# Performance work log

Hardware: AMD Instinct MI355X
Metric: run time of the kernel (lower is better)

Reference implementation:

```python
import jax, jax.numpy as jnp
import numpy as np

N_NODES, N_EDGES, F_IN, HID, N_CLASSES = 50000, 800000, 128, 128, 10
HEADS, D_HEAD, N_GRAPHS, N_CONV = 4, 32, 256, 3
BN_EPS = 1e-5
NEG_SLOPE = 0.2


def batchnorm(x, g, b):
    # training-mode BN: batch mean / biased variance over dim 0
    m = x.mean(axis=0)
    v = x.var(axis=0)
    return (x - m) * jax.lax.rsqrt(v + BN_EPS) * g + b


def segment_softmax(logits, seg, n):
    # numerically stable softmax over edges grouped by destination node
    m = jax.ops.segment_max(logits, seg, num_segments=n)
    e = jnp.exp(logits - m[seg])
    s = jax.ops.segment_sum(e, seg, num_segments=n)
    return e / (s[seg] + 1e-16)


def gat_conv(x, src, dst, W, a_src, a_dst, bias):
    # PyG GATConv (concat=True), eval mode (no attention dropout)
    n = x.shape[0]
    h = (x @ W).reshape(n, HEADS, D_HEAD)                 # [N,H,Dh]
    al_s = jnp.einsum('nhd,hd->nh', h, a_src)             # alpha from source
    al_d = jnp.einsum('nhd,hd->nh', h, a_dst)             # alpha from dest
    logits = jax.nn.leaky_relu(al_s[src] + al_d[dst], NEG_SLOPE)   # [E,H]
    alpha = segment_softmax(logits, dst, n)                # softmax over incoming edges
    msg = h[src] * alpha[:, :, None]                       # [E,H,Dh]
    out = jax.ops.segment_sum(msg, dst, num_segments=n)    # [N,H,Dh]
    return out.reshape(n, HEADS * D_HEAD) + bias


def setup_inputs() -> dict:
    key = jax.random.key(0)
    ks = jax.random.split(key, 12)
    s = 0.05
    inp = {
        'x': jax.random.normal(ks[0], (N_NODES, F_IN), dtype=jnp.float32),
        'edge_index': jax.random.randint(ks[1], (2, N_EDGES), 0, N_NODES, dtype=jnp.int32),
        'batch': jnp.sort(jax.random.randint(ks[2], (N_NODES,), 0, N_GRAPHS, dtype=jnp.int32)),
        # GCNConv(gfn=True): plain weight, no bias used
        'w_feat': s * jax.random.normal(ks[3], (F_IN, HID), dtype=jnp.float32),
        'bnf_g': jnp.ones((F_IN,), jnp.float32),
        'bnf_b': jnp.full((F_IN,), 1e-4, jnp.float32),
        'bnc_g': jnp.ones((N_CONV, HID), jnp.float32),
        'bnc_b': jnp.full((N_CONV, HID), 1e-4, jnp.float32),
        'gat_w': s * jax.random.normal(ks[4], (N_CONV, HID, HID), dtype=jnp.float32),
        'gat_asrc': s * jax.random.normal(ks[5], (N_CONV, HEADS, D_HEAD), dtype=jnp.float32),
        'gat_adst': s * jax.random.normal(ks[6], (N_CONV, HEADS, D_HEAD), dtype=jnp.float32),
        'gat_b': jnp.zeros((N_CONV, HID), jnp.float32),
        'bnfc_g': jnp.ones((HID,), jnp.float32),
        'bnfc_b': jnp.full((HID,), 1e-4, jnp.float32),
        'lin_w': s * jax.random.normal(ks[7], (HID, HID), dtype=jnp.float32),
        'lin_b': jnp.zeros((HID,), jnp.float32),
        'bnh_g': jnp.ones((HID,), jnp.float32),
        'bnh_b': jnp.full((HID,), 1e-4, jnp.float32),
        'cls_w': s * jax.random.normal(ks[8], (HID, N_CLASSES), dtype=jnp.float32),
        'cls_b': jnp.zeros((N_CLASSES,), jnp.float32),
    }
    return inp


def reference(x, edge_index, batch, w_feat, bnf_g, bnf_b, bnc_g, bnc_b,
              gat_w, gat_asrc, gat_adst, gat_b, bnfc_g, bnfc_b,
              lin_w, lin_b, bnh_g, bnh_b, cls_w, cls_b):
    n = x.shape[0]
    loops = jnp.arange(n, dtype=edge_index.dtype)
    src = jnp.concatenate([edge_index[0], loops])   # self-loops (PyG GATConv default)
    dst = jnp.concatenate([edge_index[1], loops])

    h = jax.nn.relu(batchnorm(x, bnf_g, bnf_b) @ w_feat)   # bn_feat + gfn GCNConv + relu
    for i in range(N_CONV):
        h = batchnorm(h, bnc_g[i], bnc_b[i])
        h = jax.nn.relu(gat_conv(h, src, dst, gat_w[i], gat_asrc[i], gat_adst[i], gat_b[i]))

    g = jax.ops.segment_sum(h, batch, num_segments=N_GRAPHS)   # global_add_pool [G,HID]
    g = jax.nn.relu(batchnorm(g, bnfc_g, bnfc_b) @ lin_w + lin_b)
    g = batchnorm(g, bnh_g, bnh_b)
    # dropout inactive in eval mode
    return jax.nn.log_softmax(g @ cls_w + cls_b, axis=-1)
```

## Files before the change

### kernel.cpp

```cpp
#include <hip/hip_runtime.h>
#include <math.h>

#define N_NODES 50000
#define N_EDGES 800000
#define NGRAPHS 256
#define NCONV 3
#define SCAT_CHUNK 2048
#define DMAX 64

typedef _Float16 h4 __attribute__((ext_vector_type(4)));
typedef _Float16 h8 __attribute__((ext_vector_type(8)));
typedef float f32x4 __attribute__((ext_vector_type(4)));

static inline int divup(int a, int b) { return (a + b - 1) / b; }

#define SB_CONV 0
#define SB_H2 2048
#define SB_X 2304
#define SB_TOT 2560

#define NSCAT_BLOCKS 3128

__global__ void init_kernel(float* __restrict__ SB, int* __restrict__ cursor,
                            int* __restrict__ col, int n) {
    int i = blockIdx.x * blockDim.x + threadIdx.x;
    if (i < SB_TOT) SB[i] = 0.f;
    if (i < n) {
        cursor[i] = 1;
        col[(size_t)i * DMAX] = i;
    }
}

__global__ __launch_bounds__(256) void scatter_cast(const int* __restrict__ src,
                                                    const int* __restrict__ dst,
                                                    int* __restrict__ cursor,
                                                    int* __restrict__ col, int E,
                                                    const float* __restrict__ x,
                                                    _Float16* __restrict__ y, int n,
                                                    float* __restrict__ sums) {
    if ((int)blockIdx.x < NSCAT_BLOCKS) {
        int slice = blockIdx.x & 7;
        int base = (blockIdx.x >> 3) * SCAT_CHUNK;
        int lim = min(base + SCAT_CHUNK, E);
        int lo = slice * (N_NODES / 8);
        int hi = lo + (N_NODES / 8);
        for (int i = base + threadIdx.x; i < lim; i += 256) {
            int d = dst[i];
            if (d >= lo && d < hi) {
                int p = atomicAdd(&cursor[d], 1);
                if (p < DMAX) col[(size_t)d * DMAX + p] = src[i];
            }
        }
        return;
    }
    __shared__ float S[16][128], S2[16][128];
    int bid = blockIdx.x - NSCAT_BLOCKS;
    int tid = threadIdx.x;
    int c8 = (tid & 15) * 8;
    int rg = tid >> 4;
    float s[8] = {}, s2[8] = {};
    for (int r = bid * 16 + rg; r < n; r += 256 * 16) {
        const float4* p = (const float4*)&x[(size_t)r * 128 + c8];
        float4 v0 = p[0], v1 = p[1];
        float f[8] = {v0.x, v0.y, v0.z, v0.w, v1.x, v1.y, v1.z, v1.w};
        h8 o;
#pragma unroll
        for (int i = 0; i < 8; ++i) {
            o[i] = (_Float16)f[i];
            s[i] += f[i];
            s2[i] += f[i] * f[i];
        }
        *(h8*)&y[(size_t)r * 128 + c8] = o;
    }
#pragma unroll
    for (int i = 0; i < 8; ++i) { S[rg][c8 + i] = s[i]; S2[rg][c8 + i] = s2[i]; }
    __syncthreads();
    if (tid < 128) {
        float a = 0.f, b = 0.f;
#pragma unroll
        for (int k = 0; k < 16; ++k) { a += S[k][tid]; b += S2[k][tid]; }
        atomicAdd(&sums[tid], a);
        atomicAdd(&sums[128 + tid], b);
    }
}

__global__ __launch_bounds__(256) void colstats_h(const _Float16* __restrict__ x, int n,
                                                  float* __restrict__ sums) {
    __shared__ float S[16][128], S2[16][128];
    int tid = threadIdx.x;
    int c8 = (tid & 15) * 8;
    int rg = tid >> 4;
    float s[8] = {}, s2[8] = {};
    for (int r = blockIdx.x * 16 + rg; r < n; r += gridDim.x * 16) {
        h8 v = *(const h8*)&x[(size_t)r * 128 + c8];
#pragma unroll
        for (int i = 0; i < 8; ++i) {
            float f = (float)v[i];
            s[i] += f;
            s2[i] += f * f;
        }
    }
#pragma unroll
    for (int i = 0; i < 8; ++i) { S[rg][c8 + i] = s[i]; S2[rg][c8 + i] = s2[i]; }
    __syncthreads();
    if (tid < 128) {
        float a = 0.f, b = 0.f;
#pragma unroll
        for (int k = 0; k < 16; ++k) { a += S[k][tid]; b += S2[k][tid]; }
        atomicAdd(&sums[(blockIdx.x & 7) * 256 + tid], a);
        atomicAdd(&sums[(blockIdx.x & 7) * 256 + 128 + tid], b);
    }
}

__global__ __launch_bounds__(128) void fold_t(const float* __restrict__ sums, int nsl,
                                              float inv_n,
                                              const float* __restrict__ gamma,
                                              const float* __restrict__ beta,
                                              const float* __restrict__ W,
                                              _Float16* __restrict__ WTh, float* __restrict__ bp) {
    int j = blockIdx.x, k = threadIdx.x;
    float s1 = 0.f, s2v = 0.f;
    for (int s = 0; s < nsl; ++s) { s1 += sums[s * 256 + k]; s2v += sums[s * 256 + 128 + k]; }
    float mean = s1 * inv_n;
    float var = s2v * inv_n - mean * mean;
    float sc = gamma[k] * rsqrtf(var + 1e-5f);
    float t = beta[k] - mean * sc;
    float w = W[k * 128 + j];
    WTh[j * 128 + k] = (_Float16)(sc * w);
    float pb = t * w;
    for (int off = 1; off < 64; off <<= 1) pb += __shfl_xor(pb, off, 64);
    __shared__ float r2[2];
    if ((k & 63) == 0) r2[k >> 6] = pb;
    __syncthreads();
    if (k == 0) bp[j] = r2[0] + r2[1];
}

__global__ __launch_bounds__(256) void gemm_mfma(const _Float16* __restrict__ Ah,
                                                 const _Float16* __restrict__ WTh,
                                                 const float* __restrict__ bp,
                                                 _Float16* __restrict__ outh, int n, int relu,
                                                 const float* __restrict__ asrc,
                                                 const float* __restrict__ adst,
                                                 float* __restrict__ als,
                                                 float* __restrict__ ald,
                                                 float* __restrict__ stats8,
                                                 float* __restrict__ sums_zero,
                                                 float* __restrict__ g_zero) {
    __shared__ _Float16 Wl[128 * 136];
    __shared__ float SSm[4 * 128], SS2m[4 * 128];
    int tid = threadIdx.x;
    if (sums_zero && blockIdx.x < 8) sums_zero[blockIdx.x * 256 + tid] = 0.f;
    if (g_zero && blockIdx.x < 128) g_zero[blockIdx.x * 256 + tid] = 0.f;
    for (int i = tid; i < 2048; i += 256) {
        int r = i >> 4, s = i & 15;
        *(h8*)&Wl[r * 136 + s * 8] = *(const h8*)&WTh[r * 128 + s * 8];
    }
    __syncthreads();
    int lane = tid & 63, wid = tid >> 6;
    int m = lane & 15, quad = lane >> 4;
    int rbase = blockIdx.x * 64 + wid * 16;
    bool act = rbase < n;
    const bool do_al = (asrc != nullptr);
    const bool do_st = (stats8 != nullptr);
    float st[8] = {}, s2t[8] = {};
    float ps[4][4] = {}, pd[4][4] = {};

    if (act) {
        const _Float16* arow = Ah + (size_t)(rbase + m) * 128 + quad * 8;
        h8 af0 = *(const h8*)(arow);
        h8 af1 = *(const h8*)(arow + 32);
        h8 af2 = *(const h8*)(arow + 64);
        h8 af3 = *(const h8*)(arow + 96);
#pragma unroll
        for (int t = 0; t < 8; ++t) {
            const _Float16* wrow = &Wl[(t * 16 + m) * 136 + quad * 8];
            f32x4 acc = {0.f, 0.f, 0.f, 0.f};
            acc = __builtin_amdgcn_mfma_f32_16x16x32_f16(af0, *(const h8*)(wrow), acc, 0, 0, 0);
            acc = __builtin_amdgcn_mfma_f32_16x16x32_f16(af1, *(const h8*)(wrow + 32), acc, 0, 0, 0);
            acc = __builtin_amdgcn_mfma_f32_16x16x32_f16(af2, *(const h8*)(wrow + 64), acc, 0, 0, 0);
            acc = __builtin_amdgcn_mfma_f32_16x16x32_f16(af3, *(const h8*)(wrow + 96), acc, 0, 0, 0);
            int j = t * 16 + m;
            float bj = bp[j];
            float avs = 0.f, avd = 0.f;
            if (do_al) { avs = asrc[j]; avd = adst[j]; }
            int hh = t >> 1;
#pragma unroll
            for (int r = 0; r < 4; ++r) {
                float o = acc[r] + bj;
                if (do_al) {
                    ps[r][hh] += o * avs;
                    pd[r][hh] += o * avd;
                }
                float v = relu ? fmaxf(o, 0.f) : o;
                _Float16 hv16 = (_Float16)v;
                int row = rbase + quad * 4 + r;
                outh[(size_t)row * 128 + j] = hv16;
                if (do_st) {
                    float fv = (float)hv16;
                    st[t] += fv;
                    s2t[t] += fv * fv;
                }
            }
        }
        if (do_al) {
#pragma unroll
            for (int r = 0; r < 4; ++r) {
#pragma unroll
                for (int hh = 0; hh < 4; ++hh) {
                    float v = ps[r][hh];
                    v += __shfl_xor(v, 1, 64); v += __shfl_xor(v, 2, 64);
                    v += __shfl_xor(v, 4, 64); v += __shfl_xor(v, 8, 64);
                    float w = pd[r][hh];
                    w += __shfl_xor(w, 1, 64); w += __shfl_xor(w, 2, 64);
                    w += __shfl_xor(w, 4, 64); w += __shfl_xor(w, 8, 64);
                    if (m == 0) {
                        int row = rbase + quad * 4 + r;
                        als[row * 4 + hh] = v;
                        ald[row * 4 + hh] = w;
                    }
                }
            }
        }
    }
    if (do_st) {
#pragma unroll
        for (int t = 0; t < 8; ++t) {
            st[t] += __shfl_xor(st[t], 16, 64);  st[t] += __shfl_xor(st[t], 32, 64);
            s2t[t] += __shfl_xor(s2t[t], 16, 64); s2t[t] += __shfl_xor(s2t[t], 32, 64);
        }
        if (quad == 0) {
#pragma unroll
            for (int t = 0; t < 8; ++t) {
                SSm[wid * 128 + t * 16 + m] = st[t];
                SS2m[wid * 128 + t * 16 + m] = s2t[t];
            }
        }
        __syncthreads();
        int c = tid & 127, which = tid >> 7;
        const float* A = which ? SS2m : SSm;
        float tot = A[c] + A[128 + c] + A[256 + c] + A[384 + c];
        atomicAdd(&stats8[(blockIdx.x & 7) * 256 + which * 128 + c], tot);
    }
}

__device__ __forceinline__ float leaky(float x) { return fmaxf(x, 0.2f * x); }

__global__ __launch_bounds__(256) void gat_aggregate(const _Float16* __restrict__ hp,
                                                     const float* __restrict__ al_s,
                                                     const float* __restrict__ al_d,
                                                     const int* __restrict__ cnt_arr,
                                                     const int* __restrict__ col,
                                                     const float* __restrict__ bias,
                                                     _Float16* __restrict__ h_out, int n) {
    int tid = threadIdx.x;
    int lane = tid & 63, wid = tid >> 6;
    int node = blockIdx.x * 4 + wid;
    int beg = node * DMAX;
    int end = beg + min(cnt_arr[node], DMAX);
    int q = lane >> 4, l4 = lane & 15;
    int head = l4 >> 2;
    int f0 = l4 * 8;
    float adh = al_d[node * 4 + head];
    float ch = leaky(adh);
    const _Float16* hpf = hp + f0;
    int last = end - 1;
    float ws = 0.f;
    float a0 = 0.f, a1 = 0.f, a2 = 0.f, a3 = 0.f, a4 = 0.f, a5 = 0.f, a6 = 0.f, a7 = 0.f;
    for (int e = beg + q; e < end; e += 16) {
        int e1 = e + 4, e2 = e + 8, e3 = e + 12;
        bool v1 = e1 < end, v2 = e2 < end, v3 = e3 < end;
        unsigned s0 = (unsigned)col[e];
        unsigned s1 = (unsigned)col[v1 ? e1 : last];
        unsigned s2 = (unsigned)col[v2 ? e2 : last];
        unsigned s3 = (unsigned)col[v3 ? e3 : last];
        float as0 = al_s[s0 * 4 + head];
        float as1 = al_s[s1 * 4 + head];
        float as2 = al_s[s2 * 4 + head];
        float as3 = al_s[s3 * 4 + head];
        h8 hv0 = *(const h8*)(hpf + (size_t)s0 * 128);
        h8 hv1 = *(const h8*)(hpf + (size_t)s1 * 128);
        h8 hv2 = *(const h8*)(hpf + (size_t)s2 * 128);
        h8 hv3 = *(const h8*)(hpf + (size_t)s3 * 128);
        float w0 = __expf(fminf(leaky(as0 + adh) - ch, 10.f));
        float w1 = v1 ? __expf(fminf(leaky(as1 + adh) - ch, 10.f)) : 0.f;
        float w2 = v2 ? __expf(fminf(leaky(as2 + adh) - ch, 10.f)) : 0.f;
        float w3 = v3 ? __expf(fminf(leaky(as3 + adh) - ch, 10.f)) : 0.f;
        ws += (w0 + w1) + (w2 + w3);
        a0 += (float)hv0[0] * w0 + (float)hv1[0] * w1 + (float)hv2[0] * w2 + (float)hv3[0] * w3;
        a1 += (float)hv0[1] * w0 + (float)hv1[1] * w1 + (float)hv2[1] * w2 + (float)hv3[1] * w3;
        a2 += (float)hv0[2] * w0 + (float)hv1[2] * w1 + (float)hv2[2] * w2 + (float)hv3[2] * w3;
        a3 += (float)hv0[3] * w0 + (float)hv1[3] * w1 + (float)hv2[3] * w2 + (float)hv3[3] * w3;
        a4 += (float)hv0[4] * w0 + (float)hv1[4] * w1 + (float)hv2[4] * w2 + (float)hv3[4] * w3;
        a5 += (float)hv0[5] * w0 + (float)hv1[5] * w1 + (float)hv2[5] * w2 + (float)hv3[5] * w3;
        a6 += (float)hv0[6] * w0 + (float)hv1[6] * w1 + (float)hv2[6] * w2 + (float)hv3[6] * w3;
        a7 += (float)hv0[7] * w0 + (float)hv1[7] * w1 + (float)hv2[7] * w2 + (float)hv3[7] * w3;
    }
#pragma unroll
    for (int off = 16; off <= 32; off <<= 1) {
        ws += __shfl_xor(ws, off, 64);
        a0 += __shfl_xor(a0, off, 64); a1 += __shfl_xor(a1, off, 64);
        a2 += __shfl_xor(a2, off, 64); a3 += __shfl_xor(a3, off, 64);
        a4 += __shfl_xor(a4, off, 64); a5 += __shfl_xor(a5, off, 64);
        a6 += __shfl_xor(a6, off, 64); a7 += __shfl_xor(a7, off, 64);
    }
    if (q == 0) {
        float inv = 1.f / (ws + 1e-16f);
        float4 b0 = *(const float4*)&bias[f0];
        float4 b1 = *(const float4*)&bias[f0 + 4];
        h8 ov;
        ov[0] = (_Float16)fmaxf(a0 * inv + b0.x, 0.f);
        ov[1] = (_Float16)fmaxf(a1 * inv + b0.y, 0.f);
        ov[2] = (_Float16)fmaxf(a2 * inv + b0.z, 0.f);
        ov[3] = (_Float16)fmaxf(a3 * inv + b0.w, 0.f);
        ov[4] = (_Float16)fmaxf(a4 * inv + b1.x, 0.f);
        ov[5] = (_Float16)fmaxf(a5 * inv + b1.y, 0.f);
        ov[6] = (_Float16)fmaxf(a6 * inv + b1.z, 0.f);
        ov[7] = (_Float16)fmaxf(a7 * inv + b1.w, 0.f);
        *(h8*)&h_out[(size_t)node * 128 + f0] = ov;
    }
}

__global__ void pool_kernel(const _Float16* __restrict__ h, const int* __restrict__ batch,
                            float* __restrict__ g, int n, int chunk) {
    int f = threadIdx.x;
    int a = blockIdx.x * chunk;
    if (a >= n) return;
    int b = min(n, a + chunk);
    float acc = 0.f;
    int cur = batch[a];
    for (int i = a; i < b; ++i) {
        int bi = batch[i];
        if (bi != cur) {
            atomicAdd(&g[cur * 128 + f], acc);
            acc = 0.f;
            cur = bi;
        }
        acc += (float)h[(size_t)i * 128 + f];
    }
    atomicAdd(&g[cur * 128 + f], acc);
}

__global__ __launch_bounds__(256) void gemm128_bn(const float* __restrict__ A,
                                                  const float* __restrict__ W,
                                                  const float* __restrict__ bias,
                                                  float inv_n,
                                                  const float* __restrict__ gamma,
                                                  const float* __restrict__ beta,
                                                  float* __restrict__ out,
                                                  float* __restrict__ outstats, int n) {
    __shared__ float Wl[128 * 128];
    __shared__ float hT[128 * 32];
    __shared__ float S[16][128], S2[16][128];
    __shared__ float sS[128], tS[128];
    int tid = threadIdx.x;
    for (int i = tid; i < 4096; i += 256) {
        ((float4*)Wl)[i] = ((const float4*)W)[i];
    }
    {
        int c8 = (tid & 15) * 8;
        int rg = tid >> 4;
        float s[8] = {}, s2[8] = {};
        for (int r = rg; r < n; r += 16) {
            const float4* p = (const float4*)&A[(size_t)r * 128 + c8];
            float4 v0 = p[0], v1 = p[1];
            float f[8] = {v0.x, v0.y, v0.z, v0.w, v1.x, v1.y, v1.z, v1.w};
#pragma unroll
            for (int i = 0; i < 8; ++i) { s[i] += f[i]; s2[i] += f[i] * f[i]; }
        }
#pragma unroll
        for (int i = 0; i < 8; ++i) { S[rg][c8 + i] = s[i]; S2[rg][c8 + i] = s2[i]; }
    }
    __syncthreads();
    if (tid < 128) {
        float a = 0.f, b2 = 0.f;
#pragma unroll
        for (int k = 0; k < 16; ++k) { a += S[k][tid]; b2 += S2[k][tid]; }
        float m = a * inv_n;
        float var = b2 * inv_n - m * m;
        float sc = gamma[tid] * rsqrtf(var + 1e-5f);
        sS[tid] = sc;
        tS[tid] = beta[tid] - m * sc;
    }
    __syncthreads();
    int base = blockIdx.x * 32;
    for (int pass = 0; pass < 4; ++pass) {
        int r = (tid >> 5) + pass * 8;
        int c4 = tid & 31;
        int row = base + r;
        float4 v = (row < n) ? ((const float4*)(A + (size_t)row * 128))[c4]
                             : make_float4(0.f, 0.f, 0.f, 0.f);
        int c0 = c4 * 4;
        hT[(c0 + 0) * 32 + r] = v.x * sS[c0 + 0] + tS[c0 + 0];
        hT[(c0 + 1) * 32 + r] = v.y * sS[c0 + 1] + tS[c0 + 1];
        hT[(c0 + 2) * 32 + r] = v.z * sS[c0 + 2] + tS[c0 + 2];
        hT[(c0 + 3) * 32 + r] = v.w * sS[c0 + 3] + tS[c0 + 3];
    }
    __syncthreads();
    int tx = tid & 31, ty = tid >> 5;
    int j0 = tx * 4, r0 = ty * 4;
    float acc[4][4] = {};
#pragma unroll 8
    for (int k = 0; k < 128; ++k) {
        float4 a = *(const float4*)&hT[k * 32 + r0];
        float4 w = *(const float4*)&Wl[k * 128 + j0];
        acc[0][0] += a.x * w.x; acc[0][1] += a.x * w.y; acc[0][2] += a.x * w.z; acc[0][3] += a.x * w.w;
        acc[1][0] += a.y * w.x; acc[1][1] += a.y * w.y; acc[1][2] += a.y * w.z; acc[1][3] += a.y * w.w;
        acc[2][0] += a.z * w.x; acc[2][1] += a.z * w.y; acc[2][2] += a.z * w.z; acc[2][3] += a.z * w.w;
        acc[3][0] += a.w * w.x; acc[3][1] += a.w * w.y; acc[3][2] += a.w * w.z; acc[3][3] += a.w * w.w;
    }
    float4 bb = *(const float4*)&bias[j0];
    float csum[4] = {}, csq[4] = {};
    for (int i2 = 0; i2 < 4; ++i2) {
        int row = base + r0 + i2;
        if (row < n) {
            float o0 = fmaxf(acc[i2][0] + bb.x, 0.f);
            float o1 = fmaxf(acc[i2][1] + bb.y, 0.f);
            float o2 = fmaxf(acc[i2][2] + bb.z, 0.f);
            float o3 = fmaxf(acc[i2][3] + bb.w, 0.f);
            *(float4*)&out[(size_t)row * 128 + j0] = make_float4(o0, o1, o2, o3);
            csum[0] += o0; csum[1] += o1; csum[2] += o2; csum[3] += o3;
            csq[0] += o0 * o0; csq[1] += o1 * o1; csq[2] += o2 * o2; csq[3] += o3 * o3;
        }
    }
#pragma unroll
    for (int c = 0; c < 4; ++c) {
        atomicAdd(&outstats[j0 + c], csum[c]);
        atomicAdd(&outstats[128 + j0 + c], csq[c]);
    }
}

__global__ __launch_bounds__(64) void final_kernel(const float* __restrict__ g2,
                                                   const float* __restrict__ stats, float inv_n,
                                                   const float* __restrict__ gamma,
                                                   const float* __restrict__ beta,
                                                   const float* __restrict__ W,
                                                   const float* __restrict__ b,
                                                   float* __restrict__ out, int rows) {
    int r = blockIdx.x;
    if (r >= rows) return;
    int lane = threadIdx.x;
    float logit[10] = {};
    for (int k = lane; k < 128; k += 64) {
        float m = stats[k] * inv_n;
        float var = stats[128 + k] * inv_n - m * m;
        float sc = gamma[k] * rsqrtf(var + 1e-5f);
        float gv = (g2[r * 128 + k] - m) * sc + beta[k];
#pragma unroll
        for (int j = 0; j < 10; ++j) logit[j] += gv * W[k * 10 + j];
    }
#pragma unroll
    for (int j = 0; j < 10; ++j)
        for (int off = 1; off < 64; off <<= 1) logit[j] += __shfl_xor(logit[j], off, 64);
    if (lane == 0) {
        float m = -1e30f;
#pragma unroll
        for (int j = 0; j < 10; ++j) { logit[j] += b[j]; m = fmaxf(m, logit[j]); }
        float sum = 0.f;
#pragma unroll
        for (int j = 0; j < 10; ++j) sum += expf(logit[j] - m);
        float lse = m + logf(sum);
#pragma unroll
        for (int j = 0; j < 10; ++j) out[r * 10 + j] = logit[j] - lse;
    }
}

extern "C" void kernel_launch(void* const* d_in, const int* in_sizes, int n_in,
                              void* d_out, int out_size, void* d_ws, size_t ws_size,
                              hipStream_t stream) {
    const float* x      = (const float*)d_in[0];
    const int*   ei     = (const int*)d_in[1];
    const int*   batch  = (const int*)d_in[2];
    const float* w_feat = (const float*)d_in[3];
    const float* bnf_g  = (const float*)d_in[4];
    const float* bnf_b  = (const float*)d_in[5];
    const float* bnc_g  = (const float*)d_in[6];
    const float* bnc_b  = (const float*)d_in[7];
    const float* gat_w  = (const float*)d_in[8];
    const float* gat_as = (const float*)d_in[9];
    const float* gat_ad = (const float*)d_in[10];
    const float* gat_b  = (const float*)d_in[11];
    const float* bnfc_g = (const float*)d_in[12];
    const float* bnfc_b = (const float*)d_in[13];
    const float* lin_w  = (const float*)d_in[14];
    const float* lin_b  = (const float*)d_in[15];
    const float* bnh_g  = (const float*)d_in[16];
    const float* bnh_b  = (const float*)d_in[17];
    const float* cls_w  = (const float*)d_in[18];
    const float* cls_b  = (const float*)d_in[19];
    float* out = (float*)d_out;

    char* ws = (char*)d_ws;
    size_t off = 0;
    auto alloc = [&](size_t bytes) -> void* {
        void* p = ws + off;
        off = (off + bytes + 255) & ~(size_t)255;
        return p;
    };
    _Float16* xh   = (_Float16*)alloc((size_t)N_NODES * 128 * 2);
    _Float16* h    = (_Float16*)alloc((size_t)N_NODES * 128 * 2);
    _Float16* hp   = (_Float16*)alloc((size_t)N_NODES * 128 * 2);
    float*    als  = (float*)alloc((size_t)N_NODES * 4 * 4);
    float*    ald  = (float*)alloc((size_t)N_NODES * 4 * 4);
    int*      curs = (int*)alloc((size_t)N_NODES * 4);
    int*      col  = (int*)alloc((size_t)N_NODES * DMAX * 4);
    float*    SB   = (float*)alloc(SB_TOT * 4);
    _Float16* WTh  = (_Float16*)alloc(128 * 128 * 2);
    float*    bp   = (float*)alloc(128 * 4);
    float*    g    = (float*)alloc(NGRAPHS * 128 * 4);
    float*    g2   = (float*)alloc(NGRAPHS * 128 * 4);

    const int* esrc = ei;
    const int* edst = ei + N_EDGES;

    init_kernel<<<divup(N_NODES, 256), 256, 0, stream>>>(SB, curs, col, N_NODES);

    scatter_cast<<<NSCAT_BLOCKS + 256, 256, 0, stream>>>(esrc, edst, curs, col, N_EDGES,
                                                         x, xh, N_NODES, SB + SB_X);

    fold_t<<<128, 128, 0, stream>>>(SB + SB_X, 1, 1.f / N_NODES, bnf_g, bnf_b, w_feat, WTh, bp);
    gemm_mfma<<<divup(N_NODES, 64), 256, 0, stream>>>(xh, WTh, bp, h, N_NODES, 1,
                                                      nullptr, nullptr, nullptr, nullptr,
                                                      SB + SB_CONV, nullptr, nullptr);

    for (int i = 0; i < NCONV; ++i) {
        fold_t<<<128, 128, 0, stream>>>(SB + SB_CONV, 8, 1.f / N_NODES,
                                        bnc_g + 128 * i, bnc_b + 128 * i,
                                        gat_w + 16384 * i, WTh, bp);
        gemm_mfma<<<divup(N_NODES, 64), 256, 0, stream>>>(h, WTh, bp, hp, N_NODES, 0,
                                                          gat_as + 128 * i, gat_ad + 128 * i,
                                                          als, ald, nullptr, SB + SB_CONV,
                                                          (i == 2) ? g : nullptr);
        gat_aggregate<<<N_NODES / 4, 256, 0, stream>>>(hp, als, ald, curs, col,
                                                       gat_b + 128 * i, h, N_NODES);
        if (i < NCONV - 1)
            colstats_h<<<256, 256, 0, stream>>>(h, N_NODES, SB + SB_CONV);
    }

    pool_kernel<<<divup(N_NODES, 32), 128, 0, stream>>>(h, batch, g, N_NODES, 32);
    gemm128_bn<<<divup(NGRAPHS, 32), 256, 0, stream>>>(g, lin_w, lin_b, 1.f / NGRAPHS,
                                                       bnfc_g, bnfc_b, g2, SB + SB_H2, NGRAPHS);
    final_kernel<<<NGRAPHS, 64, 0, stream>>>(g2, SB + SB_H2, 1.f / NGRAPHS, bnh_g, bnh_b,
                                             cls_w, cls_b, out, NGRAPHS);
}
```

Baseline: 372.6 us.

## Move edge scatter into first GEMM launch and shrink column indices to 16-bit

Edge-bucketing scatter blocks are moved out of the cast/stats kernel and appended to the first feature GEMM launch. This lets the CSR build overlap with MFMA work instead of with the bandwidth-bound cast pass. Neighbour indices are stored as unsigned short instead of int, halving the adjacency storage and the bytes read during aggregation. Node ids reach 49999, which fits in 16 bits, so the narrowing is lossless for this fixed size, but the code would break if node counts exceeded 65535.

```diff
diff --git a/kernel.cpp b/kernel.cpp
--- a/kernel.cpp
+++ b/kernel.cpp
@@ -7,6 +7,7 @@
 #define NCONV 3
 #define SCAT_CHUNK 2048
 #define DMAX 64
+#define GEMM_BLOCKS 782
 
 typedef _Float16 h4 __attribute__((ext_vector_type(4)));
 typedef _Float16 h8 __attribute__((ext_vector_type(8)));
@@ -22,44 +23,24 @@
 #define NSCAT_BLOCKS 3128
 
 __global__ void init_kernel(float* __restrict__ SB, int* __restrict__ cursor,
-                            int* __restrict__ col, int n) {
+                            unsigned short* __restrict__ col, int n) {
     int i = blockIdx.x * blockDim.x + threadIdx.x;
     if (i < SB_TOT) SB[i] = 0.f;
     if (i < n) {
         cursor[i] = 1;
-        col[(size_t)i * DMAX] = i;
-    }
-}
-
-__global__ __launch_bounds__(256) void scatter_cast(const int* __restrict__ src,
-                                                    const int* __restrict__ dst,
-                                                    int* __restrict__ cursor,
-                                                    int* __restrict__ col, int E,
-                                                    const float* __restrict__ x,
-                                                    _Float16* __restrict__ y, int n,
-                                                    float* __restrict__ sums) {
-    if ((int)blockIdx.x < NSCAT_BLOCKS) {
-        int slice = blockIdx.x & 7;
-        int base = (blockIdx.x >> 3) * SCAT_CHUNK;
-        int lim = min(base + SCAT_CHUNK, E);
-        int lo = slice * (N_NODES / 8);
-        int hi = lo + (N_NODES / 8);
-        for (int i = base + threadIdx.x; i < lim; i += 256) {
-            int d = dst[i];
-            if (d >= lo && d < hi) {
-                int p = atomicAdd(&cursor[d], 1);
-                if (p < DMAX) col[(size_t)d * DMAX + p] = src[i];
-            }
-        }
-        return;
-    }
+        col[(size_t)i * DMAX] = (unsigned short)i;
+    }
+}
+
+__global__ __launch_bounds__(256) void cast_stats(const float* __restrict__ x,
+                                                  _Float16* __restrict__ y, int n,
+                                                  float* __restrict__ sums) {
     __shared__ float S[16][128], S2[16][128];
-    int bid = blockIdx.x - NSCAT_BLOCKS;
     int tid = threadIdx.x;
     int c8 = (tid & 15) * 8;
     int rg = tid >> 4;
     float s[8] = {}, s2[8] = {};
-    for (int r = bid * 16 + rg; r < n; r += 256 * 16) {
+    for (int r = blockIdx.x * 16 + rg; r < n; r += gridDim.x * 16) {
         const float4* p = (const float4*)&x[(size_t)r * 128 + c8];
         float4 v0 = p[0], v1 = p[1];
         float f[8] = {v0.x, v0.y, v0.z, v0.w, v1.x, v1.y, v1.z, v1.w};
@@ -145,10 +126,30 @@
                                                  float* __restrict__ ald,
                                                  float* __restrict__ stats8,
                                                  float* __restrict__ sums_zero,
-                                                 float* __restrict__ g_zero) {
+                                                 float* __restrict__ g_zero,
+                                                 const int* __restrict__ s_src,
+                                                 const int* __restrict__ s_dst,
+                                                 int* __restrict__ s_cursor,
+                                                 unsigned short* __restrict__ s_col, int s_E) {
     __shared__ _Float16 Wl[128 * 136];
     __shared__ float SSm[4 * 128], SS2m[4 * 128];
     int tid = threadIdx.x;
+    if ((int)blockIdx.x >= GEMM_BLOCKS) {
+        int sb = blockIdx.x - GEMM_BLOCKS;
+        int slice = sb & 7;
+        int base = (sb >> 3) * SCAT_CHUNK;
+        int lim = min(base + SCAT_CHUNK, s_E);
+        int lo = slice * (N_NODES / 8);
+        int hi = lo + (N_NODES / 8);
+        for (int i = base + tid; i < lim; i += 256) {
+            int d = s_dst[i];
+            if (d >= lo && d < hi) {
+                int p = atomicAdd(&s_cursor[d], 1);
+                if (p < DMAX) s_col[(size_t)d * DMAX + p] = (unsigned short)s_src[i];
+            }
+        }
+        return;
+    }
     if (sums_zero && blockIdx.x < 8) sums_zero[blockIdx.x * 256 + tid] = 0.f;
     if (g_zero && blockIdx.x < 128) g_zero[blockIdx.x * 256 + tid] = 0.f;
     for (int i = tid; i < 2048; i += 256) {
@@ -249,7 +250,7 @@
                                                      const float* __restrict__ al_s,
                                                      const float* __restrict__ al_d,
                                                      const int* __restrict__ cnt_arr,
-                                                     const int* __restrict__ col,
+                                                     const unsigned short* __restrict__ col,
                                                      const float* __restrict__ bias,
                                                      _Float16* __restrict__ h_out, int n) {
     int tid = threadIdx.x;
@@ -502,7 +503,7 @@
     float*    als  = (float*)alloc((size_t)N_NODES * 4 * 4);
     float*    ald  = (float*)alloc((size_t)N_NODES * 4 * 4);
     int*      curs = (int*)alloc((size_t)N_NODES * 4);
-    int*      col  = (int*)alloc((size_t)N_NODES * DMAX * 4);
+    unsigned short* col = (unsigned short*)alloc((size_t)N_NODES * DMAX * 2);
     float*    SB   = (float*)alloc(SB_TOT * 4);
     _Float16* WTh  = (_Float16*)alloc(128 * 128 * 2);
     float*    bp   = (float*)alloc(128 * 4);
@@ -514,22 +515,23 @@
 
     init_kernel<<<divup(N_NODES, 256), 256, 0, stream>>>(SB, curs, col, N_NODES);
 
-    scatter_cast<<<NSCAT_BLOCKS + 256, 256, 0, stream>>>(esrc, edst, curs, col, N_EDGES,
-                                                         x, xh, N_NODES, SB + SB_X);
+    cast_stats<<<256, 256, 0, stream>>>(x, xh, N_NODES, SB + SB_X);
 
     fold_t<<<128, 128, 0, stream>>>(SB + SB_X, 1, 1.f / N_NODES, bnf_g, bnf_b, w_feat, WTh, bp);
-    gemm_mfma<<<divup(N_NODES, 64), 256, 0, stream>>>(xh, WTh, bp, h, N_NODES, 1,
+    gemm_mfma<<<GEMM_BLOCKS + NSCAT_BLOCKS, 256, 0, stream>>>(xh, WTh, bp, h, N_NODES, 1,
                                                       nullptr, nullptr, nullptr, nullptr,
-                                                      SB + SB_CONV, nullptr, nullptr);
+                                                      SB + SB_CONV, nullptr, nullptr,
+                                                      esrc, edst, curs, col, N_EDGES);
 
     for (int i = 0; i < NCONV; ++i) {
         fold_t<<<128, 128, 0, stream>>>(SB + SB_CONV, 8, 1.f / N_NODES,
                                         bnc_g + 128 * i, bnc_b + 128 * i,
                                         gat_w + 16384 * i, WTh, bp);
-        gemm_mfma<<<divup(N_NODES, 64), 256, 0, stream>>>(h, WTh, bp, hp, N_NODES, 0,
-                                                          gat_as + 128 * i, gat_ad + 128 * i,
-                                                          als, ald, nullptr, SB + SB_CONV,
-                                                          (i == 2) ? g : nullptr);
+        gemm_mfma<<<GEMM_BLOCKS, 256, 0, stream>>>(h, WTh, bp, hp, N_NODES, 0,
+                                                   gat_as + 128 * i, gat_ad + 128 * i,
+                                                   als, ald, nullptr, SB + SB_CONV,
+                                                   (i == 2) ? g : nullptr,
+                                                   nullptr, nullptr, nullptr, nullptr, 0);
         gat_aggregate<<<N_NODES / 4, 256, 0, stream>>>(hp, als, ald, curs, col,
                                                        gat_b + 128 * i, h, N_NODES);
         if (i < NCONV - 1)
```

Result: no change. 376.4 us (+1.0%).
